# Kernel optimization log

Measured on AMD Instinct MI355X. Metric: run time of the kernel, lower is better.

Reference implementation:

```python
import jax, jax.numpy as jnp
import numpy as np

B, T, SD, NE = 4, 2048, 64, 4096   # batch, block_size, sqrt_d, n_embd (= SD*SD)
H, HS = 8, 8                        # n_head, head_size (H*HS == SD)
FH = 4 * SD                         # FFN hidden
EPS = 1e-5


def setup_inputs() -> dict:
    key = jax.random.key(0)
    ks = jax.random.split(key, 17)
    s = 0.05  # linear-layer init scale
    return {
        "x": jax.random.normal(ks[0], (B, T, NE), jnp.float32),
        # Feebler / Booster weights: torch.randn in original
        "feebler_w": jax.random.normal(ks[1], (SD, SD, T), jnp.float32),
        "booster_w": jax.random.normal(ks[2], (SD, SD, T), jnp.float32),
        # per-head q/k/v projections (no bias): applied as y @ W -> (B,T,HS)
        "wq": jax.random.normal(ks[3], (H, SD, HS), jnp.float32) * s,
        "wk": jax.random.normal(ks[4], (H, SD, HS), jnp.float32) * s,
        "wv": jax.random.normal(ks[5], (H, SD, HS), jnp.float32) * s,
        "proj_w": jax.random.normal(ks[6], (SD, SD), jnp.float32) * s,
        "proj_b": jnp.zeros((SD,), jnp.float32),
        "ln1_g": jnp.ones((SD,), jnp.float32),
        "ln1_b": jnp.zeros((SD,), jnp.float32),
        "ln2_g": jnp.ones((SD,), jnp.float32),
        "ln2_b": jnp.zeros((SD,), jnp.float32),
        "w1": jax.random.normal(ks[7], (SD, FH), jnp.float32) * s,
        "b1": jnp.zeros((FH,), jnp.float32),
        "w2": jax.random.normal(ks[8], (FH, SD), jnp.float32) * s,
        "b2": jnp.zeros((SD,), jnp.float32),
    }


def _layer_norm(x, g, b):
    m = jnp.mean(x, axis=-1, keepdims=True)
    v = jnp.mean((x - m) ** 2, axis=-1, keepdims=True)
    return (x - m) * jax.lax.rsqrt(v + EPS) * g + b


def reference(x, feebler_w, booster_w, wq, wk, wv, proj_w, proj_b,
              ln1_g, ln1_b, ln2_g, ln2_b, w1, b1, w2, b2):
    # ---- Feebler: (B,T,NE) flat-reshaped to (B,SD,SD,T), mul weights, sum dim 2
    xr = x.reshape(B, SD, SD, T)                     # flat reinterpretation (torch .view)
    h = jnp.einsum('bijt,ijt->bit', xr, feebler_w)   # (B, SD, T)
    h = h.reshape(B, T, SD)                          # flat reinterpretation, NOT transpose

    # ---- QuickHead multi-head 'attention' (sum-pooled elementwise)
    y = _layer_norm(h, ln1_g, ln1_b)                 # (B, T, SD)
    q = jnp.einsum('bts,hsd->bhtd', y, wq)           # (B, H, T, HS)
    k = jnp.einsum('bts,hsd->bhtd', y, wk)
    v = jnp.einsum('bts,hsd->bhtd', y, wv)
    ck = jnp.sum(k, axis=2, keepdims=True)           # (B, H, 1, HS)
    cv = jnp.sum(v, axis=2, keepdims=True)
    aw = jax.nn.softmax(q * ck, axis=2)              # softmax over T
    sa = cv * aw                                     # (B, H, T, HS)
    sa = jnp.transpose(sa, (0, 2, 1, 3)).reshape(B, T, SD)  # concat heads
    sa = sa @ proj_w + proj_b                        # proj (dropout = identity, eval)
    h = h + sa

    # ---- FeedForward
    y2 = _layer_norm(h, ln2_g, ln2_b)
    f = jax.nn.relu(y2 @ w1 + b1) @ w2 + b2
    h = h + f

    # ---- Booster: broadcast-multiply against (SD,SD,T) weights
    hr = h.reshape(B, SD, T)                         # flat reinterpretation
    rev = booster_w[None, :, :, :] * hr[:, None, :, :]  # (B, SD, SD, T)
    return rev.reshape(B, T, NE)                     # flat reinterpretation
```

## Files before the change

### kernel.cpp

```cpp
#include <hip/hip_runtime.h>
#include <hip/hip_bf16.h>


#define EPSF 1e-5f
#define OFFS 40.0f

__global__ void K1(const float* __restrict__ x, const float* __restrict__ fw,
                   const float* __restrict__ g, const float* __restrict__ bia,
                   float* __restrict__ h, float* __restrict__ y,
                   float* __restrict__ part) {
    int xb = blockIdx.x;
    int b = xb & 3, i = xb >> 2;
    int t4 = blockIdx.y * 256 + threadIdx.x;
    const float4* x4 = (const float4*)x + (size_t)b * 2097152 + (size_t)i * 32768 + t4;
    const float4* f4 = (const float4*)fw + (size_t)i * 32768 + t4;
    float4 acc = make_float4(0.f, 0.f, 0.f, 0.f);
    #pragma unroll 8
    for (int j = 0; j < 64; ++j) {
        float4 xv = x4[(size_t)j * 512];
        float4 fv = f4[(size_t)j * 512];
        acc.x += xv.x * fv.x; acc.y += xv.y * fv.y;
        acc.z += xv.z * fv.z; acc.w += xv.w * fv.w;
    }
    float s1 = acc.x + acc.y + acc.z + acc.w;
    float s2 = acc.x * acc.x + acc.y * acc.y + acc.z * acc.z + acc.w * acc.w;
    for (int off = 8; off; off >>= 1) {
        s1 += __shfl_xor(s1, off);
        s2 += __shfl_xor(s2, off);
    }
    float m = s1 * (1.f / 64.f);
    float var = s2 * (1.f / 64.f) - m * m;
    float rs = rsqrtf(var + EPSF);
    float4 gv = ((const float4*)g)[t4 & 15];
    float4 bv = ((const float4*)bia)[t4 & 15];
    float4 yv;
    yv.x = (acc.x - m) * rs * gv.x + bv.x;
    yv.y = (acc.y - m) * rs * gv.y + bv.y;
    yv.z = (acc.z - m) * rs * gv.z + bv.z;
    yv.w = (acc.w - m) * rs * gv.w + bv.w;
    size_t oidx = (size_t)b * 32768 + (size_t)i * 512 + t4;
    ((float4*)h)[oidx] = acc;
    ((float4*)y)[oidx] = yv;
    __shared__ float ysL[64];
    if (threadIdx.x < 64) ysL[threadIdx.x] = 0.f;
    __syncthreads();
    int c0 = (t4 & 15) * 4;
    atomicAdd(&ysL[c0 + 0], yv.x);
    atomicAdd(&ysL[c0 + 1], yv.y);
    atomicAdd(&ysL[c0 + 2], yv.z);
    atomicAdd(&ysL[c0 + 3], yv.w);
    __syncthreads();
    if (threadIdx.x < 64)
        part[(blockIdx.y * 256 + xb) * 64 + threadIdx.x] = ysL[threadIdx.x];
}

__global__ void K1r(const float* __restrict__ part, const float* __restrict__ wk,
                    const float* __restrict__ wv, float* __restrict__ ck,
                    float* __restrict__ cv) {
    __shared__ float ysL[256];
    int tid = threadIdx.x;
    int b = tid >> 6, c = tid & 63;
    float s = 0.f;
    for (int k = 0; k < 128; ++k) {
        int i = k & 63, yy = k >> 6;
        s += part[(yy * 256 + i * 4 + b) * 64 + c];
    }
    ysL[tid] = s;
    __syncthreads();
    int hh = c >> 3, d = c & 7;
    float a = 0.f, e = 0.f;
    for (int sdx = 0; sdx < 64; ++sdx) {
        float ys = ysL[b * 64 + sdx];
        a += ys * wk[hh * 512 + sdx * 8 + d];
        e += ys * wv[hh * 512 + sdx * 8 + d];
    }
    ck[tid] = a;
    cv[tid] = e;
}

__global__ void K2(const float* __restrict__ y, const float* __restrict__ wq,
                   const float* __restrict__ ck, float* __restrict__ e,
                   float* __restrict__ esum) {
    __shared__ float yT[64][20];
    __shared__ float wqL[64][64];
    __shared__ float psum[4][64];
    int b = blockIdx.x, tile = blockIdx.y, t0 = tile * 16;
    int tid = threadIdx.x;
    for (int k = 0; k < 4; ++k) {
        int idx = k * 256 + tid;
        int r = idx >> 6, s = idx & 63;
        yT[s][r] = y[(size_t)b * 131072 + (size_t)(t0 + r) * 64 + s];
    }
    for (int k = 0; k < 16; ++k) {
        int idx = k * 256 + tid;
        int r = idx >> 6, cc = idx & 63;
        wqL[r][cc] = wq[(cc >> 3) * 512 + r * 8 + (cc & 7)];
    }
    __syncthreads();
    int c = tid & 63, tq = tid >> 6;
    float ckc = ck[b * 64 + c];
    float acc[4] = {0.f, 0.f, 0.f, 0.f};
    for (int s = 0; s < 64; ++s) {
        float w = wqL[s][c];
        float4 a0 = *(const float4*)&yT[s][tq * 4];
        acc[0] += a0.x * w; acc[1] += a0.y * w;
        acc[2] += a0.z * w; acc[3] += a0.w * w;
    }
    float ls = 0.f;
    #pragma unroll
    for (int k = 0; k < 4; ++k) {
        float v = __expf(acc[k] * ckc - OFFS);
        e[(size_t)b * 131072 + (size_t)(t0 + tq * 4 + k) * 64 + c] = v;
        ls += v;
    }
    psum[tq][c] = ls;
    __syncthreads();
    if (tid < 64)
        esum[(b * 128 + tile) * 64 + tid] =
            psum[0][tid] + psum[1][tid] + psum[2][tid] + psum[3][tid];
}

__global__ void K4(const float* __restrict__ h, const float* __restrict__ e,
                   const float* __restrict__ esum, const float* __restrict__ cv,
                   const float* __restrict__ projw, const float* __restrict__ projb,
                   const float* __restrict__ g2, const float* __restrict__ b2l,
                   const float* __restrict__ w1, const float* __restrict__ b1,
                   const float* __restrict__ w2, const float* __restrict__ fb2,
                   const float* __restrict__ bw, float* __restrict__ out) {
    __shared__ float2 pT[4][64];
    __shared__ float2 y2T[4][64];
    __shared__ float2 hidT[4][256];
    __shared__ float hfL[512];
    int b = blockIdx.x, chunk = blockIdx.y;
    int tid = threadIdx.x, l = tid & 63, w = tid >> 6;

    float den = 0.f;
    for (int t = 0; t < 128; ++t) den += esum[(b * 128 + t) * 64 + l];
    float scl = cv[b * 64 + l] / den;
    size_t base = (size_t)b * 131072 + (size_t)(chunk * 8 + w * 2) * 64 + l;

    float2 p;
    p.x = e[base] * scl;
    p.y = e[base + 64] * scl;
    pT[w][l] = p;
    __syncthreads();

    float a0 = 0.f, a1 = 0.f;
    for (int c = 0; c < 64; ++c) {
        float2 pv = pT[w][c];
        float pw = projw[c * 64 + l];
        a0 += pv.x * pw; a1 += pv.y * pw;
    }
    float pb = projb[l], g2v = g2[l], b2v = b2l[l];
    float hmid[2], y2[2];
    hmid[0] = h[base] + a0 + pb;
    hmid[1] = h[base + 64] + a1 + pb;
    #pragma unroll
    for (int rr = 0; rr < 2; ++rr) {
        float v = hmid[rr];
        float s1 = v, s2 = v * v;
        for (int off = 32; off; off >>= 1) {
            s1 += __shfl_xor(s1, off);
            s2 += __shfl_xor(s2, off);
        }
        float mm = s1 * (1.f / 64.f);
        float var = s2 * (1.f / 64.f) - mm * mm;
        float rs = rsqrtf(var + EPSF);
        y2[rr] = (v - mm) * rs * g2v + b2v;
    }
    y2T[w][l] = make_float2(y2[0], y2[1]);
    __syncthreads();

    float h1[4][2];
    #pragma unroll
    for (int u = 0; u < 4; ++u) {
        float bb = b1[u * 64 + l];
        h1[u][0] = bb; h1[u][1] = bb;
    }
    for (int s = 0; s < 64; ++s) {
        float2 yv = y2T[w][s];
        #pragma unroll
        for (int u = 0; u < 4; ++u) {
            float w1v = w1[s * 256 + u * 64 + l];
            h1[u][0] += yv.x * w1v;
            h1[u][1] += yv.y * w1v;
        }
    }
    #pragma unroll
    for (int u = 0; u < 4; ++u)
        hidT[w][u * 64 + l] = make_float2(fmaxf(h1[u][0], 0.f), fmaxf(h1[u][1], 0.f));
    __syncthreads();

    float c0 = 0.f, c1 = 0.f;
    #pragma unroll 4
    for (int jj = 0; jj < 256; ++jj) {
        float2 hv = hidT[w][jj];
        float w2v = w2[jj * 64 + l];
        c0 += hv.x * w2v; c1 += hv.y * w2v;
    }
    float fb = fb2[l];
    hfL[(w * 2 + 0) * 64 + l] = hmid[0] + c0 + fb;
    hfL[(w * 2 + 1) * 64 + l] = hmid[1] + c1 + fb;
    __syncthreads();

    int jj = chunk >> 2;
    int tq4 = (chunk & 3) * 128;
    int f4 = tid & 127, ig = tid >> 7;
    float4 hv = *(const float4*)&hfL[f4 * 4];
    const float4* bwp = (const float4*)bw + (size_t)jj * 512 + tq4 + f4;
    float4* op = (float4*)out + (size_t)b * 2097152 + (size_t)jj * 512 + tq4 + f4;
    for (int it = 0; it < 32; ++it) {
        int i = it * 2 + ig;
        float4 wv = bwp[(size_t)i * 32768];
        float4 ov;
        ov.x = wv.x * hv.x; ov.y = wv.y * hv.y;
        ov.z = wv.z * hv.z; ov.w = wv.w * hv.w;
        op[(size_t)i * 32768] = ov;
    }
}

extern "C" void kernel_launch(void* const* d_in, const int* in_sizes, int n_in,
                              void* d_out, int out_size, void* d_ws, size_t ws_size,
                              hipStream_t stream) {
    const float* x     = (const float*)d_in[0];
    const float* fw    = (const float*)d_in[1];
    const float* bw    = (const float*)d_in[2];
    const float* wq    = (const float*)d_in[3];
    const float* wk    = (const float*)d_in[4];
    const float* wv    = (const float*)d_in[5];
    const float* projw = (const float*)d_in[6];
    const float* projb = (const float*)d_in[7];
    const float* g1    = (const float*)d_in[8];
    const float* b1l   = (const float*)d_in[9];
    const float* g2    = (const float*)d_in[10];
    const float* b2l   = (const float*)d_in[11];
    const float* w1    = (const float*)d_in[12];
    const float* b1    = (const float*)d_in[13];
    const float* w2    = (const float*)d_in[14];
    const float* b2    = (const float*)d_in[15];
    float* out = (float*)d_out;

    float* wsf = (float*)d_ws;
    float* h    = wsf;
    float* y    = wsf + 524288;
    float* e    = wsf + 1048576;
    float* part = wsf + 1572864;
    float* esum = wsf + 1605632;
    float* ck   = wsf + 1638400;
    float* cvb  = wsf + 1638656;

    K1 <<<dim3(256, 2), 256, 0, stream>>>(x, fw, g1, b1l, h, y, part);
    K1r<<<1, 256, 0, stream>>>(part, wk, wv, ck, cvb);
    K2 <<<dim3(4, 128), 256, 0, stream>>>(y, wq, ck, e, esum);
    K4 <<<dim3(4, 256), 256, 0, stream>>>(h, e, esum, cvb, projw, projb,
                                          g2, b2l, w1, b1, w2, b2, bw, out);
}
```

Before: 140.5 us.

## Stage FFN and proj weights in LDS, fuse FFN chunks, precompute softmax scale

Moves the per-block softmax denominator reduction into a separate tiny kernel (K2r) that writes one scale per (batch, channel), so the 1024 K4 blocks no longer each sum 128 partials. Inside K4, the proj, w1 and w2 weights are staged through shared memory in 64-column chunks. The two FFN matmuls are fused chunk by chunk, so the hidden buffer shrinks and global weight reads are coalesced. This adds an extra launch, more barriers and about 34KB of LDS per block, which can limit occupancy.

```diff
diff --git a/kernel.cpp b/kernel.cpp
--- a/kernel.cpp
+++ b/kernel.cpp
@@ -120,41 +120,54 @@
             psum[0][tid] + psum[1][tid] + psum[2][tid] + psum[3][tid];
 }
 
-__global__ void K4(const float* __restrict__ h, const float* __restrict__ e,
-                   const float* __restrict__ esum, const float* __restrict__ cv,
-                   const float* __restrict__ projw, const float* __restrict__ projb,
-                   const float* __restrict__ g2, const float* __restrict__ b2l,
-                   const float* __restrict__ w1, const float* __restrict__ b1,
-                   const float* __restrict__ w2, const float* __restrict__ fb2,
-                   const float* __restrict__ bw, float* __restrict__ out) {
+__global__ void K2r(const float* __restrict__ esum, const float* __restrict__ cv,
+                    float* __restrict__ scl) {
+    int tid = threadIdx.x;
+    int b = tid >> 6, l = tid & 63;
+    float s = 0.f;
+    for (int t = 0; t < 128; ++t) s += esum[(b * 128 + t) * 64 + l];
+    scl[tid] = cv[tid] / s;
+}
+
+__global__ void __launch_bounds__(256, 4)
+K4(const float* __restrict__ h, const float* __restrict__ e,
+   const float* __restrict__ scl, const float* __restrict__ projw,
+   const float* __restrict__ projb, const float* __restrict__ g2,
+   const float* __restrict__ b2l, const float* __restrict__ w1,
+   const float* __restrict__ b1, const float* __restrict__ w2,
+   const float* __restrict__ fb2, const float* __restrict__ bw,
+   float* __restrict__ out) {
+    __shared__ float bufA[4096];
+    __shared__ float bufB[4096];
     __shared__ float2 pT[4][64];
     __shared__ float2 y2T[4][64];
-    __shared__ float2 hidT[4][256];
+    __shared__ float2 hidT[4][64];
     __shared__ float hfL[512];
     int b = blockIdx.x, chunk = blockIdx.y;
     int tid = threadIdx.x, l = tid & 63, w = tid >> 6;
 
-    float den = 0.f;
-    for (int t = 0; t < 128; ++t) den += esum[(b * 128 + t) * 64 + l];
-    float scl = cv[b * 64 + l] / den;
+    #pragma unroll
+    for (int k = 0; k < 16; ++k) bufA[k * 256 + tid] = projw[k * 256 + tid];
+
+    float sc = scl[b * 64 + l];
     size_t base = (size_t)b * 131072 + (size_t)(chunk * 8 + w * 2) * 64 + l;
-
     float2 p;
-    p.x = e[base] * scl;
-    p.y = e[base + 64] * scl;
+    p.x = e[base] * sc;
+    p.y = e[base + 64] * sc;
     pT[w][l] = p;
+    float h0 = h[base], hh1 = h[base + 64];
     __syncthreads();
 
     float a0 = 0.f, a1 = 0.f;
     for (int c = 0; c < 64; ++c) {
         float2 pv = pT[w][c];
-        float pw = projw[c * 64 + l];
+        float pw = bufA[c * 64 + l];
         a0 += pv.x * pw; a1 += pv.y * pw;
     }
     float pb = projb[l], g2v = g2[l], b2v = b2l[l];
     float hmid[2], y2[2];
-    hmid[0] = h[base] + a0 + pb;
-    hmid[1] = h[base + 64] + a1 + pb;
+    hmid[0] = h0 + a0 + pb;
+    hmid[1] = hh1 + a1 + pb;
     #pragma unroll
     for (int rr = 0; rr < 2; ++rr) {
         float v = hmid[rr];
@@ -171,36 +184,36 @@
     y2T[w][l] = make_float2(y2[0], y2[1]);
     __syncthreads();
 
-    float h1[4][2];
-    #pragma unroll
-    for (int u = 0; u < 4; ++u) {
-        float bb = b1[u * 64 + l];
-        h1[u][0] = bb; h1[u][1] = bb;
-    }
-    for (int s = 0; s < 64; ++s) {
-        float2 yv = y2T[w][s];
+    float a2_0 = 0.f, a2_1 = 0.f;
+    for (int c4 = 0; c4 < 4; ++c4) {
         #pragma unroll
-        for (int u = 0; u < 4; ++u) {
-            float w1v = w1[s * 256 + u * 64 + l];
-            h1[u][0] += yv.x * w1v;
-            h1[u][1] += yv.y * w1v;
-        }
-    }
-    #pragma unroll
-    for (int u = 0; u < 4; ++u)
-        hidT[w][u * 64 + l] = make_float2(fmaxf(h1[u][0], 0.f), fmaxf(h1[u][1], 0.f));
-    __syncthreads();
-
-    float c0 = 0.f, c1 = 0.f;
-    #pragma unroll 4
-    for (int jj = 0; jj < 256; ++jj) {
-        float2 hv = hidT[w][jj];
-        float w2v = w2[jj * 64 + l];
-        c0 += hv.x * w2v; c1 += hv.y * w2v;
+        for (int k = 0; k < 16; ++k) {
+            int idx = k * 256 + tid;
+            int r = idx >> 6, jc = idx & 63;
+            bufA[idx] = w1[r * 256 + c4 * 64 + jc];
+            bufB[idx] = w2[(c4 * 64 + r) * 64 + jc];
+        }
+        __syncthreads();
+        float bb = b1[c4 * 64 + l];
+        float hc0 = bb, hc1 = bb;
+        for (int s = 0; s < 64; ++s) {
+            float2 yv = y2T[w][s];
+            float w1v = bufA[s * 64 + l];
+            hc0 += yv.x * w1v;
+            hc1 += yv.y * w1v;
+        }
+        hidT[w][l] = make_float2(fmaxf(hc0, 0.f), fmaxf(hc1, 0.f));
+        for (int j = 0; j < 64; ++j) {
+            float2 hv = hidT[w][j];
+            float w2v = bufB[j * 64 + l];
+            a2_0 += hv.x * w2v;
+            a2_1 += hv.y * w2v;
+        }
+        __syncthreads();
     }
     float fb = fb2[l];
-    hfL[(w * 2 + 0) * 64 + l] = hmid[0] + c0 + fb;
-    hfL[(w * 2 + 1) * 64 + l] = hmid[1] + c1 + fb;
+    hfL[(w * 2 + 0) * 64 + l] = hmid[0] + a2_0 + fb;
+    hfL[(w * 2 + 1) * 64 + l] = hmid[1] + a2_1 + fb;
     __syncthreads();
 
     int jj = chunk >> 2;
@@ -248,10 +261,12 @@
     float* esum = wsf + 1605632;
     float* ck   = wsf + 1638400;
     float* cvb  = wsf + 1638656;
+    float* scl  = wsf + 1638912;
 
     K1 <<<dim3(256, 2), 256, 0, stream>>>(x, fw, g1, b1l, h, y, part);
     K1r<<<1, 256, 0, stream>>>(part, wk, wv, ck, cvb);
     K2 <<<dim3(4, 128), 256, 0, stream>>>(y, wq, ck, e, esum);
-    K4 <<<dim3(4, 256), 256, 0, stream>>>(h, e, esum, cvb, projw, projb,
+    K2r<<<1, 256, 0, stream>>>(esum, cvb, scl);
+    K4 <<<dim3(4, 256), 256, 0, stream>>>(h, e, scl, projw, projb,
                                           g2, b2l, w1, b1, w2, b2, bw, out);
 }
```

New measurement: 146.2 us. +4.1%, slower.
